# Performance work log

Measured on AMD Instinct MI355X. Metric: run time of the kernel, lower is better.

## Reference

```python
import jax, jax.numpy as jnp
import numpy as np

NUM_TOKENS = 128
STRING_SIZE = 512
HIDDEN_SIZE = 2048
L_IN = 256
L_OUT = 256
MAX_PROGRAM_LENGTH = 10


def _lstm_scan(xs, h, c, Wih, Whh, b):
    """Run a PyTorch-convention LSTM (gate order i,f,g,o) over xs [L, D]."""
    def step(carry, x):
        h, c = carry
        g = x @ Wih.T + h @ Whh.T + b          # [4H]
        i, f, gg, o = jnp.split(g, 4)
        c2 = jax.nn.sigmoid(f) * c + jax.nn.sigmoid(i) * jnp.tanh(gg)
        h2 = jax.nn.sigmoid(o) * jnp.tanh(c2)
        return (h2, c2), None
    (h, c), _ = jax.lax.scan(step, (h, c), xs)
    return h, c


def setup_inputs() -> dict:
    key = jax.random.key(0)
    ks = jax.random.split(key, 13)
    H, S = HIDDEN_SIZE, STRING_SIZE
    def p(k, shape, scale=0.02):
        return scale * jax.random.normal(k, shape, dtype=jnp.float32)
    return {
        "input_sequence": jax.random.randint(ks[0], (L_IN,), 0, NUM_TOKENS),
        "output_sequence": jax.random.randint(ks[1], (L_OUT,), 0, NUM_TOKENS),
        "embed": p(ks[2], (NUM_TOKENS, S), 1.0),
        "eos": p(ks[3], (S,), 1.0),
        "in_Wih": p(ks[4], (4 * H, S)), "in_Whh": p(ks[5], (4 * H, H)), "in_b": p(ks[6], (4 * H,)),
        "out_Wih": p(ks[7], (4 * H, S)), "out_Whh": p(ks[8], (4 * H, H)), "out_b": p(ks[9], (4 * H,)),
        "prog_Wih": p(ks[10], (4 * H, H)), "prog_Whh": p(ks[11], (4 * H, H)), "prog_b": p(ks[12], (4 * H,)),
    }


def reference(input_sequence, output_sequence, embed, eos,
              in_Wih, in_Whh, in_b, out_Wih, out_Whh, out_b,
              prog_Wih, prog_Whh, prog_b):
    H = in_Whh.shape[1]
    h = jnp.zeros((H,), embed.dtype)
    c = jnp.zeros((H,), embed.dtype)
    # encode input string (+ end-of-sequence token) with input_lstm
    xs_in = jnp.concatenate([embed[input_sequence], eos[None]], axis=0)   # [L_in+1, S]
    h, c = _lstm_scan(xs_in, h, c, in_Wih, in_Whh, in_b)
    # encode output string (+ eos) with output_lstm, state carried over
    xs_out = jnp.concatenate([embed[output_sequence], eos[None]], axis=0)  # [L_out+1, S]
    h, c = _lstm_scan(xs_out, h, c, out_Wih, out_Whh, out_b)
    def prog_step(carry, _):
        h, c = carry
        g = h @ prog_Wih.T + h @ prog_Whh.T + prog_b
        i, f, gg, o = jnp.split(g, 4)
        c2 = jax.nn.sigmoid(f) * c + jax.nn.sigmoid(i) * jnp.tanh(gg)
        h2 = jax.nn.sigmoid(o) * jnp.tanh(c2)
        return (h2, c2), h2
    _, prog = jax.lax.scan(prog_step, (h, c), None, length=MAX_PROGRAM_LENGTH)
    return prog  # [MAX_PROGRAM_LENGTH, H] (stack of program hidden states)
```

## Files before the change

kernel.cpp:

```cpp
#include <hip/hip_runtime.h>

typedef unsigned short u16;
typedef unsigned int u32;
typedef unsigned long long u64;

#define NBLK 256

__device__ __forceinline__ float b2f(u16 u) {
    u32 i = ((u32)u) << 16;
    return __builtin_bit_cast(float, i);
}
__device__ __forceinline__ u16 f2b(float f) {
    u32 b = __builtin_bit_cast(u32, f);
    b += 0x7FFFu + ((b >> 16) & 1u);
    return (u16)(b >> 16);
}
__device__ __forceinline__ float sigm(float x) {
    return 1.f / (1.f + __expf(-x));
}
__device__ __forceinline__ float tanh_fast(float x) {
    float a = fabsf(x);
    float e = __expf(-2.f * a);
    float r = (1.f - e) / (1.f + e);
    return copysignf(r, x);
}

__global__ void __launch_bounds__(256)
xproj_kernel(const float* __restrict__ embed, const float* __restrict__ eos,
             const int* __restrict__ seqA, const int* __restrict__ seqB,
             const float* __restrict__ WA, const float* __restrict__ WB,
             const float* __restrict__ bA, const float* __restrict__ bB,
             float* __restrict__ XpA, float* __restrict__ XpB)
{
    __shared__ float xs[8][512];
    const int which = blockIdx.x >> 8;
    const int bx = blockIdx.x & 255;
    const int* __restrict__ seq  = which ? seqB : seqA;
    const float* __restrict__ W  = which ? WB : WA;
    const float* __restrict__ bias = which ? bB : bA;
    float* __restrict__ Xp = which ? XpB : XpA;

    const int tid = threadIdx.x;
    const int t0 = blockIdx.y * 8;
    const int nt = min(8, 257 - t0);

    for (int idx = tid; idx < nt * 512; idx += 256) {
        int tt = idx >> 9, col = idx & 511;
        int t = t0 + tt;
        xs[tt][col] = (t < 256) ? embed[(size_t)seq[t] * 512 + col] : eos[col];
    }
    __syncthreads();

    const int lane = tid & 63;
    const int wv = tid >> 6;

    float xr[8][8];
#pragma unroll
    for (int tt = 0; tt < 8; ++tt) {
        *(float4*)&xr[tt][0] = *(const float4*)&xs[tt][lane * 8];
        *(float4*)&xr[tt][4] = *(const float4*)&xs[tt][lane * 8 + 4];
    }

#pragma unroll 1
    for (int rr = 0; rr < 8; ++rr) {
        int r = bx * 32 + wv * 8 + rr;
        float wf[8];
        *(float4*)&wf[0] = *(const float4*)&W[(size_t)r * 512 + lane * 8];
        *(float4*)&wf[4] = *(const float4*)&W[(size_t)r * 512 + lane * 8 + 4];
        float acc[8];
#pragma unroll
        for (int tt = 0; tt < 8; tt++) {
            float a = 0.f;
#pragma unroll
            for (int j = 0; j < 8; j++) a = fmaf(wf[j], xr[tt][j], a);
            acc[tt] = a;
        }
#pragma unroll
        for (int tt = 0; tt < 8; tt++) {
            float a = acc[tt];
#pragma unroll
            for (int off = 32; off > 0; off >>= 1) a += __shfl_xor(a, off, 64);
            if (lane == 0 && tt < nt) {
                int g = r >> 11, rem = r & 2047, wgi = rem >> 3, j = rem & 7;
                Xp[(size_t)(t0 + tt) * 8192 + (wgi << 5) + (g << 3) + j] = a + bias[r];
            }
        }
    }
}

__global__ void __launch_bounds__(512, 1)
rnn_coop(const float* __restrict__ WhhA, const float* __restrict__ WhhB,
         const float* __restrict__ pWih, const float* __restrict__ pWhh,
         const float* __restrict__ pB,
         const float* __restrict__ Xp0, const float* __restrict__ Xp1,
         u32* __restrict__ hseqB, float* __restrict__ out)
{
    __shared__ __align__(16) float hs[2048];
    __shared__ float gsum[32];

    const int wg = blockIdx.x;
    const int tid = threadIdx.x;
    const int lane = tid & 63;
    const int wv = tid >> 6;

    float w[4][32];
    float c_reg = 0.f;

    if (tid < 32) gsum[tid] = 0.f;

    float xp_cur = 0.f, xp_nxt = 0.f;
    if (wv == 0 && lane < 32)
        xp_cur = Xp0[(size_t)0 * 8192 + (wg << 5) + lane];

    for (int t = 0; t < 524; ++t) {
        const int phase = (t < 257) ? 0 : (t < 514) ? 1 : 2;

        if (t == 0 || t == 257 || t == 514) {
            if (phase < 2) {
                const float* Ws = phase ? WhhB : WhhA;
#pragma unroll
                for (int rr = 0; rr < 4; ++rr) {
                    int rl = (wv << 2) + rr;
                    const float* Wr = Ws + (size_t)(((rl >> 3) << 11) + (wg << 3) + (rl & 7)) * 2048;
#pragma unroll
                    for (int q = 0; q < 8; ++q)
                        *(float4*)&w[rr][q * 4] = *(const float4*)&Wr[(q << 8) + (lane << 2)];
                }
            } else {
#pragma unroll
                for (int rr = 0; rr < 4; ++rr) {
                    int rl = (wv << 2) + rr;
                    size_t off = (size_t)(((rl >> 3) << 11) + (wg << 3) + (rl & 7)) * 2048;
#pragma unroll
                    for (int q = 0; q < 8; ++q) {
                        float4 a = *(const float4*)&pWih[off + (q << 8) + (lane << 2)];
                        float4 b = *(const float4*)&pWhh[off + (q << 8) + (lane << 2)];
                        float4 s;
                        s.x = a.x + b.x; s.y = a.y + b.y;
                        s.z = a.z + b.z; s.w = a.w + b.w;
                        *(float4*)&w[rr][q * 4] = s;
                    }
                }
            }
        }

        if (t > 0) {
            const u64* src = (const u64*)hseqB + (size_t)(t - 1) * 4096
                             + ((wg & 7) << 9) + tid;
            u64 a = __hip_atomic_load(src, __ATOMIC_RELAXED, __HIP_MEMORY_SCOPE_AGENT);
            while ((u16)a == 0xFFFFu || (u16)(a >> 16) == 0xFFFFu ||
                   (u16)(a >> 32) == 0xFFFFu || (u16)(a >> 48) == 0xFFFFu)
                a = __hip_atomic_load(src, __ATOMIC_RELAXED, __HIP_MEMORY_SCOPE_AGENT);
            float4 hv;
            hv.x = b2f((u16)a);         hv.y = b2f((u16)(a >> 16));
            hv.z = b2f((u16)(a >> 32)); hv.w = b2f((u16)(a >> 48));
            *(float4*)&hs[tid << 2] = hv;
        }
        __syncthreads();

        if (wv == 0 && lane < 32 && t < 523) {
            const int tn = t + 1;
            if (tn < 257)       xp_nxt = Xp0[(size_t)tn * 8192 + (wg << 5) + lane];
            else if (tn < 514)  xp_nxt = Xp1[(size_t)(tn - 257) * 8192 + (wg << 5) + lane];
            else                xp_nxt = pB[((lane >> 3) << 11) + (wg << 3) + (lane & 7)];
        }

        if (t > 0) {
            float a0 = 0.f, a1 = 0.f, a2 = 0.f, a3 = 0.f;
#pragma unroll
            for (int q = 0; q < 8; ++q) {
                float4 hv = *(const float4*)&hs[(q << 8) + (lane << 2)];
#pragma unroll
                for (int j = 0; j < 4; ++j) {
                    float h = ((const float*)&hv)[j];
                    a0 = fmaf(w[0][q * 4 + j], h, a0);
                    a1 = fmaf(w[1][q * 4 + j], h, a1);
                    a2 = fmaf(w[2][q * 4 + j], h, a2);
                    a3 = fmaf(w[3][q * 4 + j], h, a3);
                }
            }
#pragma unroll
            for (int off = 32; off > 0; off >>= 1) {
                a0 += __shfl_xor(a0, off, 64);
                a1 += __shfl_xor(a1, off, 64);
                a2 += __shfl_xor(a2, off, 64);
                a3 += __shfl_xor(a3, off, 64);
            }
            if (lane == 0) {
                const int rl = wv << 2;
                gsum[rl]     = a0;
                gsum[rl + 1] = a1;
                gsum[rl + 2] = a2;
                gsum[rl + 3] = a3;
            }
        }
        __syncthreads();

        if (wv == 0) {
            float tot = xp_cur + gsum[lane & 31];
            float act = ((lane >> 3) == 2) ? tanh_fast(tot) : sigm(tot);
            const int j = lane & 7;
            float fi = __shfl(act, j, 64);
            float ff = __shfl(act, 8 + j, 64);
            float fg = __shfl(act, 16 + j, 64);
            float fo = __shfl(act, 24 + j, 64);
            c_reg = ff * c_reg + fi * fg;
            float h2 = fo * tanh_fast(c_reg);
            u32 hb = (u32)f2b(h2);
            u32 lo = (u32)__shfl((int)hb, (lane & 3) * 2, 64);
            u32 hi = (u32)__shfl((int)hb, (lane & 3) * 2 + 1, 64);
            if (lane < 32)
                __hip_atomic_store(&hseqB[(size_t)t * 8192 + ((lane >> 2) << 10)
                                          + (wg << 2) + (lane & 3)],
                                   (hi << 16) | lo,
                                   __ATOMIC_RELAXED, __HIP_MEMORY_SCOPE_AGENT);
            if (phase == 2 && lane < 8)
                out[(size_t)(t - 514) * 2048 + (wg << 3) + lane] = h2;
        }
        xp_cur = xp_nxt;
    }
}

extern "C" void kernel_launch(void* const* d_in, const int* in_sizes, int n_in,
                              void* d_out, int out_size, void* d_ws, size_t ws_size,
                              hipStream_t stream) {
    const int*   in_seq   = (const int*)d_in[0];
    const int*   out_seq  = (const int*)d_in[1];
    const float* embed    = (const float*)d_in[2];
    const float* eos      = (const float*)d_in[3];
    const float* in_Wih   = (const float*)d_in[4];
    const float* in_Whh   = (const float*)d_in[5];
    const float* in_b     = (const float*)d_in[6];
    const float* out_Wih  = (const float*)d_in[7];
    const float* out_Whh  = (const float*)d_in[8];
    const float* out_b    = (const float*)d_in[9];
    const float* pg_Wih   = (const float*)d_in[10];
    const float* pg_Whh   = (const float*)d_in[11];
    const float* pg_b     = (const float*)d_in[12];

    float* Xp0   = (float*)d_ws;
    float* Xp1   = Xp0 + (size_t)257 * 8192;
    u32*   hseqB = (u32*)(Xp1 + (size_t)257 * 8192);

    hipMemsetAsync(hseqB, 0xFF, (size_t)524 * 8192 * sizeof(u32), stream);

    dim3 g1(512, 33), b1(256);
    hipLaunchKernelGGL(xproj_kernel, g1, b1, 0, stream, embed, eos,
                       in_seq, out_seq, in_Wih, out_Wih, in_b, out_b, Xp0, Xp1);

    float* out = (float*)d_out;
    void* args[] = { (void*)&in_Whh, (void*)&out_Whh, (void*)&pg_Wih, (void*)&pg_Whh,
                     (void*)&pg_b, (void*)&Xp0, (void*)&Xp1, (void*)&hseqB, (void*)&out };
    hipLaunchCooperativeKernel((const void*)rnn_coop, dim3(NBLK), dim3(512),
                               args, 0, stream);
}
```

Before: 2.019 ms.

## Read hidden state directly into registers per wave, drop LDS staging and barrier

```diff
diff --git a/kernel.cpp b/kernel.cpp
--- a/kernel.cpp
+++ b/kernel.cpp
@@ -61,12 +61,20 @@
         *(float4*)&xr[tt][4] = *(const float4*)&xs[tt][lane * 8 + 4];
     }
 
+    float wf[8];
+    {
+        const int r = bx * 32 + wv * 8;
+        *(float4*)&wf[0] = *(const float4*)&W[(size_t)r * 512 + lane * 8];
+        *(float4*)&wf[4] = *(const float4*)&W[(size_t)r * 512 + lane * 8 + 4];
+    }
 #pragma unroll 1
     for (int rr = 0; rr < 8; ++rr) {
-        int r = bx * 32 + wv * 8 + rr;
-        float wf[8];
-        *(float4*)&wf[0] = *(const float4*)&W[(size_t)r * 512 + lane * 8];
-        *(float4*)&wf[4] = *(const float4*)&W[(size_t)r * 512 + lane * 8 + 4];
+        const int r = bx * 32 + wv * 8 + rr;
+        float wfn[8];
+        if (rr < 7) {
+            *(float4*)&wfn[0] = *(const float4*)&W[(size_t)(r + 1) * 512 + lane * 8];
+            *(float4*)&wfn[4] = *(const float4*)&W[(size_t)(r + 1) * 512 + lane * 8 + 4];
+        }
         float acc[8];
 #pragma unroll
         for (int tt = 0; tt < 8; tt++) {
@@ -84,6 +92,10 @@
                 int g = r >> 11, rem = r & 2047, wgi = rem >> 3, j = rem & 7;
                 Xp[(size_t)(t0 + tt) * 8192 + (wgi << 5) + (g << 3) + j] = a + bias[r];
             }
+        }
+        if (rr < 7) {
+#pragma unroll
+            for (int j = 0; j < 8; ++j) wf[j] = wfn[j];
         }
     }
 }
@@ -93,9 +105,8 @@
          const float* __restrict__ pWih, const float* __restrict__ pWhh,
          const float* __restrict__ pB,
          const float* __restrict__ Xp0, const float* __restrict__ Xp1,
-         u32* __restrict__ hseqB, float* __restrict__ out)
+         u64* __restrict__ hseq64, float* __restrict__ out)
 {
-    __shared__ __align__(16) float hs[2048];
     __shared__ float gsum[32];
 
     const int wg = blockIdx.x;
@@ -105,15 +116,38 @@
 
     float w[4][32];
     float c_reg = 0.f;
+    float xp2 = 0.f;
 
     if (tid < 32) gsum[tid] = 0.f;
 
     float xp_cur = 0.f, xp_nxt = 0.f;
     if (wv == 0 && lane < 32)
-        xp_cur = Xp0[(size_t)0 * 8192 + (wg << 5) + lane];
+        xp_cur = Xp0[(wg << 5) + lane];
 
     for (int t = 0; t < 524; ++t) {
         const int phase = (t < 257) ? 0 : (t < 514) ? 1 : 2;
+
+        u64 v[8];
+        if (t > 0) {
+            const u64* src = hseq64 + (size_t)(t - 1) * 512;
+#pragma unroll
+            for (int q = 0; q < 8; ++q)
+                v[q] = __hip_atomic_load(&src[(q << 6) + lane], __ATOMIC_RELAXED,
+                                         __HIP_MEMORY_SCOPE_AGENT);
+            for (;;) {
+                u32 m = 0;
+#pragma unroll
+                for (int q = 0; q < 8; ++q)
+                    if (v[q] == ~0ull) m |= 1u << q;
+                if (!__any(m != 0)) break;
+#pragma unroll
+                for (int q = 0; q < 8; ++q)
+                    if (m & (1u << q))
+                        v[q] = __hip_atomic_load(&src[(q << 6) + lane],
+                                                 __ATOMIC_RELAXED,
+                                                 __HIP_MEMORY_SCOPE_AGENT);
+            }
+        }
 
         if (t == 0 || t == 257 || t == 514) {
             if (phase < 2) {
@@ -141,43 +175,42 @@
                         *(float4*)&w[rr][q * 4] = s;
                     }
                 }
-            }
-        }
-
-        if (t > 0) {
-            const u64* src = (const u64*)hseqB + (size_t)(t - 1) * 4096
-                             + ((wg & 7) << 9) + tid;
-            u64 a = __hip_atomic_load(src, __ATOMIC_RELAXED, __HIP_MEMORY_SCOPE_AGENT);
-            while ((u16)a == 0xFFFFu || (u16)(a >> 16) == 0xFFFFu ||
-                   (u16)(a >> 32) == 0xFFFFu || (u16)(a >> 48) == 0xFFFFu)
-                a = __hip_atomic_load(src, __ATOMIC_RELAXED, __HIP_MEMORY_SCOPE_AGENT);
-            float4 hv;
-            hv.x = b2f((u16)a);         hv.y = b2f((u16)(a >> 16));
-            hv.z = b2f((u16)(a >> 32)); hv.w = b2f((u16)(a >> 48));
-            *(float4*)&hs[tid << 2] = hv;
-        }
-        __syncthreads();
+                if (wv == 0 && lane < 32)
+                    xp2 = pB[((lane >> 3) << 11) + (wg << 3) + (lane & 7)];
+            }
+        }
 
         if (wv == 0 && lane < 32 && t < 523) {
             const int tn = t + 1;
             if (tn < 257)       xp_nxt = Xp0[(size_t)tn * 8192 + (wg << 5) + lane];
             else if (tn < 514)  xp_nxt = Xp1[(size_t)(tn - 257) * 8192 + (wg << 5) + lane];
-            else                xp_nxt = pB[((lane >> 3) << 11) + (wg << 3) + (lane & 7)];
         }
 
         if (t > 0) {
             float a0 = 0.f, a1 = 0.f, a2 = 0.f, a3 = 0.f;
 #pragma unroll
             for (int q = 0; q < 8; ++q) {
-                float4 hv = *(const float4*)&hs[(q << 8) + (lane << 2)];
-#pragma unroll
-                for (int j = 0; j < 4; ++j) {
-                    float h = ((const float*)&hv)[j];
-                    a0 = fmaf(w[0][q * 4 + j], h, a0);
-                    a1 = fmaf(w[1][q * 4 + j], h, a1);
-                    a2 = fmaf(w[2][q * 4 + j], h, a2);
-                    a3 = fmaf(w[3][q * 4 + j], h, a3);
-                }
+                const u64 a = v[q];
+                const float h0 = b2f((u16)a);
+                const float h1 = b2f((u16)(a >> 16));
+                const float h2v = b2f((u16)(a >> 32));
+                const float h3 = b2f((u16)(a >> 48));
+                a0 = fmaf(w[0][q * 4 + 0], h0, a0);
+                a1 = fmaf(w[1][q * 4 + 0], h0, a1);
+                a2 = fmaf(w[2][q * 4 + 0], h0, a2);
+                a3 = fmaf(w[3][q * 4 + 0], h0, a3);
+                a0 = fmaf(w[0][q * 4 + 1], h1, a0);
+                a1 = fmaf(w[1][q * 4 + 1], h1, a1);
+                a2 = fmaf(w[2][q * 4 + 1], h1, a2);
+                a3 = fmaf(w[3][q * 4 + 1], h1, a3);
+                a0 = fmaf(w[0][q * 4 + 2], h2v, a0);
+                a1 = fmaf(w[1][q * 4 + 2], h2v, a1);
+                a2 = fmaf(w[2][q * 4 + 2], h2v, a2);
+                a3 = fmaf(w[3][q * 4 + 2], h2v, a3);
+                a0 = fmaf(w[0][q * 4 + 3], h3, a0);
+                a1 = fmaf(w[1][q * 4 + 3], h3, a1);
+                a2 = fmaf(w[2][q * 4 + 3], h3, a2);
+                a3 = fmaf(w[3][q * 4 + 3], h3, a3);
             }
 #pragma unroll
             for (int off = 32; off > 0; off >>= 1) {
@@ -197,7 +230,8 @@
         __syncthreads();
 
         if (wv == 0) {
-            float tot = xp_cur + gsum[lane & 31];
+            float xpv = (phase < 2) ? xp_cur : xp2;
+            float tot = xpv + gsum[lane & 31];
             float act = ((lane >> 3) == 2) ? tanh_fast(tot) : sigm(tot);
             const int j = lane & 7;
             float fi = __shfl(act, j, 64);
@@ -207,12 +241,14 @@
             c_reg = ff * c_reg + fi * fg;
             float h2 = fo * tanh_fast(c_reg);
             u32 hb = (u32)f2b(h2);
-            u32 lo = (u32)__shfl((int)hb, (lane & 3) * 2, 64);
-            u32 hi = (u32)__shfl((int)hb, (lane & 3) * 2 + 1, 64);
-            if (lane < 32)
-                __hip_atomic_store(&hseqB[(size_t)t * 8192 + ((lane >> 2) << 10)
-                                          + (wg << 2) + (lane & 3)],
-                                   (hi << 16) | lo,
+            const int base = (lane & 1) << 2;
+            u32 b0 = (u32)__shfl((int)hb, base + 0, 64) & 0xFFFFu;
+            u32 b1 = (u32)__shfl((int)hb, base + 1, 64) & 0xFFFFu;
+            u32 b2 = (u32)__shfl((int)hb, base + 2, 64) & 0xFFFFu;
+            u32 b3 = (u32)__shfl((int)hb, base + 3, 64) & 0xFFFFu;
+            u64 pk = (u64)(b0 | (b1 << 16)) | (((u64)(b2 | (b3 << 16))) << 32);
+            if (lane < 2)
+                __hip_atomic_store(&hseq64[(size_t)t * 512 + (wg << 1) + lane], pk,
                                    __ATOMIC_RELAXED, __HIP_MEMORY_SCOPE_AGENT);
             if (phase == 2 && lane < 8)
                 out[(size_t)(t - 514) * 2048 + (wg << 3) + lane] = h2;
@@ -238,11 +274,11 @@
     const float* pg_Whh   = (const float*)d_in[11];
     const float* pg_b     = (const float*)d_in[12];
 
-    float* Xp0   = (float*)d_ws;
-    float* Xp1   = Xp0 + (size_t)257 * 8192;
-    u32*   hseqB = (u32*)(Xp1 + (size_t)257 * 8192);
-
-    hipMemsetAsync(hseqB, 0xFF, (size_t)524 * 8192 * sizeof(u32), stream);
+    float* Xp0    = (float*)d_ws;
+    float* Xp1    = Xp0 + (size_t)257 * 8192;
+    u64*   hseq64 = (u64*)(Xp1 + (size_t)257 * 8192);
+
+    hipMemsetAsync(hseq64, 0xFF, (size_t)524 * 512 * sizeof(u64), stream);
 
     dim3 g1(512, 33), b1(256);
     hipLaunchKernelGGL(xproj_kernel, g1, b1, 0, stream, embed, eos,
@@ -250,7 +286,7 @@
 
     float* out = (float*)d_out;
     void* args[] = { (void*)&in_Whh, (void*)&out_Whh, (void*)&pg_Wih, (void*)&pg_Whh,
-                     (void*)&pg_b, (void*)&Xp0, (void*)&Xp1, (void*)&hseqB, (void*)&out };
+                     (void*)&pg_b, (void*)&Xp0, (void*)&Xp1, (void*)&hseq64, (void*)&out };
     hipLaunchCooperativeKernel((const void*)rnn_coop, dim3(NBLK), dim3(512),
                                args, 0, stream);
 }
```

Result: slower. 3.446 ms (+70.7%).
